# Kernel optimization log

Measured on AMD Instinct MI355X. Metric: run time of the kernel, lower is better.

## Reference

```python
import jax, jax.numpy as jnp
import numpy as np

D_MODEL = 1024
N_HEADS = 16
HEAD_DIM = D_MODEL // N_HEADS
WINDOW = 128
N_PERSIST = 4
KSIZE = 3


def _make_mask(L):
    """[T,T] additive mask, T = N_PERSIST + L. Persistent rows: causal among
    persistent tokens. Sequence rows: all persistent cols + sliding causal window."""
    T = N_PERSIST + L
    r = jnp.arange(T)[:, None]
    c = jnp.arange(T)[None, :]
    seq_allowed = (c < N_PERSIST) | ((c >= jnp.maximum(N_PERSIST, r - WINDOW + 1)) & (c <= r))
    allowed = jnp.where(r < N_PERSIST, c <= r, seq_allowed)
    return jnp.where(allowed, 0.0, -jnp.inf).astype(jnp.float32)


def _causal_dw_conv(y, w, b):
    # y: [B,T,D] -> depthwise causal conv1d + SiLU -> [B,T,D]
    y = y.transpose(0, 2, 1)  # [B,D,T]
    y = jax.lax.conv_general_dilated(
        y, w, window_strides=(1,), padding=[(KSIZE - 1, 0)],
        feature_group_count=D_MODEL, dimension_numbers=('NCH', 'OIH', 'NCH'))
    y = jax.nn.silu(y + b[None, :, None])
    return y.transpose(0, 2, 1)


def _l2norm(y, eps=1e-12):
    n = jnp.linalg.norm(y, axis=-1, keepdims=True)
    return y / jnp.maximum(n, eps)


def setup_inputs() -> dict:
    key = jax.random.key(0)
    ks = jax.random.split(key, 12)
    s = 1.0 / np.sqrt(D_MODEL)
    return {
        'x': jax.random.normal(ks[0], (1, 2048, D_MODEL), jnp.float32),
        'persistent_memory': jax.random.normal(ks[1], (1, N_PERSIST, D_MODEL), jnp.float32) * 0.02,
        'Wq': jax.random.normal(ks[2], (D_MODEL, D_MODEL), jnp.float32) * s,
        'Wk': jax.random.normal(ks[3], (D_MODEL, D_MODEL), jnp.float32) * s,
        'Wv': jax.random.normal(ks[4], (D_MODEL, D_MODEL), jnp.float32) * s,
        'Wo': jax.random.normal(ks[5], (D_MODEL, D_MODEL), jnp.float32) * s,
        'q_conv_w': jax.random.normal(ks[6], (D_MODEL, 1, KSIZE), jnp.float32) * 0.3,
        'q_conv_b': jax.random.normal(ks[7], (D_MODEL,), jnp.float32) * 0.02,
        'k_conv_w': jax.random.normal(ks[8], (D_MODEL, 1, KSIZE), jnp.float32) * 0.3,
        'k_conv_b': jax.random.normal(ks[9], (D_MODEL,), jnp.float32) * 0.02,
        'v_conv_w': jax.random.normal(ks[10], (D_MODEL, 1, KSIZE), jnp.float32) * 0.3,
        'v_conv_b': jax.random.normal(ks[11], (D_MODEL,), jnp.float32) * 0.02,
    }


def reference(x, persistent_memory, Wq, Wk, Wv, Wo,
              q_conv_w, q_conv_b, k_conv_w, k_conv_b, v_conv_w, v_conv_b):
    B, L, D = x.shape
    T = L + N_PERSIST
    scale = HEAD_DIM ** -0.5
    xp = jnp.concatenate([jnp.broadcast_to(persistent_memory, (B, N_PERSIST, D)), x], axis=1)
    Q = xp @ Wq.T
    K = xp @ Wk.T
    V = xp @ Wv.T
    Q = _causal_dw_conv(Q, q_conv_w, q_conv_b)
    K = _causal_dw_conv(K, k_conv_w, k_conv_b)
    V = _causal_dw_conv(V, v_conv_w, v_conv_b)
    Q = _l2norm(Q)
    K = _l2norm(K)
    # [B,H,T,hd]
    Q = Q.reshape(B, T, N_HEADS, HEAD_DIM).transpose(0, 2, 1, 3)
    K = K.reshape(B, T, N_HEADS, HEAD_DIM).transpose(0, 2, 1, 3)
    V = V.reshape(B, T, N_HEADS, HEAD_DIM).transpose(0, 2, 1, 3)
    scores = jnp.einsum('bhqd,bhkd->bhqk', Q, K) * scale + _make_mask(L)[None, None]
    attn = jax.nn.softmax(scores, axis=-1)
    out = jnp.einsum('bhqk,bhkd->bhqd', attn, V)
    out = out.transpose(0, 2, 1, 3).reshape(B, T, D) @ Wo.T
    return out[:, N_PERSIST:, :]
```

## Files before the change

kernel.cpp:

```cpp
#include <hip/hip_runtime.h>
#include <math.h>

typedef unsigned short u16;
typedef unsigned int   u32;
typedef unsigned long long u64;
typedef __attribute__((ext_vector_type(8))) short bf16x8;
typedef __attribute__((ext_vector_type(4))) float f32x4;
typedef __attribute__((ext_vector_type(4))) int i32x4;

#define TTOT  2052
#define NPERS 4
#define LSEQ  2048
#define WIN   128
#define NHEAD 16
#define HDIM  64
#define DM    1024
#define MPAD  2176

__device__ __forceinline__ float bf2f(u16 u) {
    union { unsigned int i; float f; } v; v.i = ((unsigned int)u) << 16; return v.f;
}
__device__ __forceinline__ u16 f2bf(float f) {
    union { float f; unsigned int i; } v; v.f = f;
    unsigned int r = (v.i + 0x7fffu + ((v.i >> 16) & 1u)) >> 16;
    return (u16)r;
}
__device__ __forceinline__ u32 pk2(float lo, float hi) {
    return (u32)f2bf(lo) | ((u32)f2bf(hi) << 16);
}

__device__ __forceinline__ void glds16(const u16* g, u16* l) {
    __builtin_amdgcn_global_load_lds(
        (__attribute__((address_space(1))) void*)(g),
        (__attribute__((address_space(3))) void*)(l),
        16, 0, 0);
}

#define XP_UNITS (TTOT * DM / 4)
#define W_UNITS  (DM * DM / 4)
#define CVT_BLOCKS ((XP_UNITS + 4 * W_UNITS) / 256)

__global__ __launch_bounds__(256) void cvt(const float* __restrict__ x, const float* __restrict__ pm,
    const float* __restrict__ Wq, const float* __restrict__ Wk, const float* __restrict__ Wv,
    const float* __restrict__ Wo,
    u16* __restrict__ xp, u16* __restrict__ Wcat, u16* __restrict__ Woh)
{
    const int id = blockIdx.x * 256 + threadIdx.x;
    const float* s; u16* d;
    if (id < XP_UNITS) {
        const size_t e = (size_t)id * 4;
        const int row = (int)(e >> 10), c = (int)(e & 1023);
        s = (row < NPERS) ? (pm + (size_t)row * DM + c) : (x + (size_t)(row - NPERS) * DM + c);
        d = xp + e;
    } else {
        const int w   = id - XP_UNITS;
        const int sel = w >> 18;
        const size_t e = (size_t)(w & (W_UNITS - 1)) * 4;
        if (sel == 0)      { s = Wq + e; d = Wcat + e; }
        else if (sel == 1) { s = Wk + e; d = Wcat + (size_t)DM * DM + e; }
        else if (sel == 2) { s = Wv + e; d = Wcat + 2 * (size_t)DM * DM + e; }
        else               { s = Wo + e; d = Woh + e; }
    }
    f32x4 v = *(const f32x4*)s;
    *(u64*)d = (u64)pk2(v[0], v[1]) | ((u64)pk2(v[2], v[3]) << 32);
}

template<int TM, int TN, bool OF32>
__device__ __forceinline__ void gemm_lds(const u16* __restrict__ Ablk, const u16* __restrict__ Bblk,
                                         void* __restrict__ Cbase, int mlim)
{
    __shared__ __align__(16) u16 As[TM * 64];
    __shared__ __align__(16) u16 Bs[TN * 64];
    const int tid  = threadIdx.x;
    const int lane = tid & 63;
    const int l15  = lane & 15, quad = lane >> 4;
    constexpr int RM = TM / 32, RN = TN / 32;
    const int wm = (tid >> 7) * (TM / 2);
    const int wn = ((tid >> 6) & 1) * (TN / 2);

    f32x4 acc[RM][RN];
    #pragma unroll
    for (int i = 0; i < RM; i++)
        #pragma unroll
        for (int j = 0; j < RN; j++) acc[i][j] = (f32x4){0.f, 0.f, 0.f, 0.f};

    constexpr int LA = TM / 32;
    constexpr int LB = TN / 32;

    for (int kk = 0; kk < DM; kk += 64) {
        #pragma unroll
        for (int i = 0; i < LA; i++) {
            const int e = i * 256 + tid;
            const int row = e >> 3, sc = (e & 7) ^ (row & 7);
            glds16(Ablk + (size_t)row * DM + kk + sc * 8, As + (size_t)e * 8);
        }
        #pragma unroll
        for (int i = 0; i < LB; i++) {
            const int e = i * 256 + tid;
            const int row = e >> 3, sc = (e & 7) ^ (row & 7);
            glds16(Bblk + (size_t)row * DM + kk + sc * 8, Bs + (size_t)e * 8);
        }
        __syncthreads();
        #pragma unroll
        for (int kc = 0; kc < 2; kc++) {
            bf16x8 af[RM], bfr[RN];
            #pragma unroll
            for (int i = 0; i < RM; i++)
                af[i]  = *(const bf16x8*)&As[(wm + i * 16 + l15) * 64 + (((kc * 4 + quad) ^ (l15 & 7)) * 8)];
            #pragma unroll
            for (int j = 0; j < RN; j++)
                bfr[j] = *(const bf16x8*)&Bs[(wn + j * 16 + l15) * 64 + (((kc * 4 + quad) ^ (l15 & 7)) * 8)];
            #pragma unroll
            for (int i = 0; i < RM; i++)
                #pragma unroll
                for (int j = 0; j < RN; j++)
                    acc[i][j] = __builtin_amdgcn_mfma_f32_16x16x32_bf16(af[i], bfr[j], acc[i][j], 0, 0, 0);
        }
        __syncthreads();
    }

    #pragma unroll
    for (int i = 0; i < RM; i++) {
        const int m0 = wm + i * 16 + quad * 4;
        #pragma unroll
        for (int j = 0; j < RN; j++) {
            const int n = wn + j * 16 + l15;
            #pragma unroll
            for (int r = 0; r < 4; r++) {
                const int m = m0 + r;
                if (m < mlim) {
                    if (OF32) ((float*)Cbase)[(size_t)m * DM + n] = acc[i][j][r];
                    else      ((u16*)Cbase)[(size_t)m * DM + n]   = f2bf(acc[i][j][r]);
                }
            }
        }
    }
}

__global__ __launch_bounds__(256) void gemm_qkv(const u16* __restrict__ xp, const u16* __restrict__ Wcat,
    u16* __restrict__ Qr, u16* __restrict__ Kr, u16* __restrict__ Vr)
{
    const int Mb = blockIdx.x * 128;
    const int nb = blockIdx.y;
    u16* C = (nb < 8) ? Qr : (nb < 16) ? Kr : Vr;
    const int Ncol = (nb & 7) * 128;
    gemm_lds<128, 128, false>(xp + (size_t)Mb * DM,
                              Wcat + (size_t)nb * 128 * DM,
                              (void*)(C + (size_t)Mb * DM + Ncol),
                              TTOT - Mb);
}

__global__ __launch_bounds__(256) void gemm_out(const u16* __restrict__ AO, const u16* __restrict__ Woh,
                                                float* __restrict__ Cout)
{
    const int Mb = blockIdx.x * 64, Nb = blockIdx.y * 128;
    gemm_lds<64, 128, true>(AO + (size_t)Mb * DM, Woh + (size_t)Nb * DM,
                            (void*)(Cout + (size_t)Mb * DM + Nb), 64);
}

__global__ __launch_bounds__(256) void conv_silu_norm(
    const u16* __restrict__ Qr, const u16* __restrict__ Kr, const u16* __restrict__ Vr,
    const float* __restrict__ qw, const float* __restrict__ qb,
    const float* __restrict__ kw, const float* __restrict__ kb,
    const float* __restrict__ vw, const float* __restrict__ vb,
    u16* __restrict__ Qc, u16* __restrict__ Kc, u16* __restrict__ Vc)
{
    const int t0 = blockIdx.x * 2;
    const int z  = blockIdx.y;
    const u16* raw; const float *w, *b; u16* out;
    if (z == 0)      { raw = Qr; w = qw; b = qb; out = Qc; }
    else if (z == 1) { raw = Kr; w = kw; b = kb; out = Kc; }
    else             { raw = Vr; w = vw; b = vb; out = Vc; }

    const int tid = threadIdx.x;
    const int d0  = tid * 4;

    const u16* r0 = raw + (size_t)t0 * DM + d0;
    const u64 cm2 = (t0 >= 2) ? *(const u64*)(r0 - 2 * DM) : 0ULL;
    const u64 cm1 = (t0 >= 1) ? *(const u64*)(r0 - DM)     : 0ULL;
    const u64 c0  = *(const u64*)r0;
    const u64 c1  = *(const u64*)(r0 + DM);
    const f32x4 bias = *(const f32x4*)(b + d0);
    const f32x4 w0v  = *(const f32x4*)(w + 3 * d0);
    const f32x4 w1v  = *(const f32x4*)(w + 3 * d0 + 4);
    const f32x4 w2v  = *(const f32x4*)(w + 3 * d0 + 8);
    const float warr[12] = {w0v[0], w0v[1], w0v[2], w0v[3],
                            w1v[0], w1v[1], w1v[2], w1v[3],
                            w2v[0], w2v[1], w2v[2], w2v[3]};

    float va[4], vb2[4];
    float ss0 = 0.f, ss1 = 0.f;
    #pragma unroll
    for (int c = 0; c < 4; c++) {
        const float xm2 = bf2f((u16)(cm2 >> (16 * c)));
        const float xm1 = bf2f((u16)(cm1 >> (16 * c)));
        const float x0  = bf2f((u16)(c0  >> (16 * c)));
        const float x1  = bf2f((u16)(c1  >> (16 * c)));
        const float w0 = warr[3*c], w1 = warr[3*c + 1], w2 = warr[3*c + 2];
        float a0 = bias[c] + w2 * x0 + w1 * xm1 + w0 * xm2;
        float a1 = bias[c] + w2 * x1 + w1 * x0  + w0 * xm1;
        const float y0 = a0 / (1.f + __expf(-a0));
        const float y1 = a1 / (1.f + __expf(-a1));
        va[c] = y0; vb2[c] = y1;
        ss0 += y0 * y0; ss1 += y1 * y1;
    }
    float inv0 = 1.f, inv1 = 1.f;
    if (z < 2) {
        #pragma unroll
        for (int off = 32; off > 0; off >>= 1) {
            ss0 += __shfl_down(ss0, off, 64);
            ss1 += __shfl_down(ss1, off, 64);
        }
        __shared__ float red[8];
        const int wv = tid >> 6, ln = tid & 63;
        if (ln == 0) { red[wv] = ss0; red[wv + 4] = ss1; }
        __syncthreads();
        inv0 = 1.f / fmaxf(sqrtf(red[0] + red[1] + red[2] + red[3]), 1e-12f);
        inv1 = 1.f / fmaxf(sqrtf(red[4] + red[5] + red[6] + red[7]), 1e-12f);
    }
    u64 o0 = 0, o1 = 0;
    #pragma unroll
    for (int c = 0; c < 4; c++) {
        o0 |= (u64)f2bf(va[c]  * inv0) << (16 * c);
        o1 |= (u64)f2bf(vb2[c] * inv1) << (16 * c);
    }
    *(u64*)(out + (size_t)t0 * DM + d0)      = o0;
    *(u64*)(out + (size_t)(t0 + 1) * DM + d0) = o1;
}

#define QT     64
#define KTILES 13
#define KROWS  208
#define KPAD   224
#define VSTR   232

__global__ __launch_bounds__(256) void attn(const u16* __restrict__ Q, const u16* __restrict__ K,
                                            const u16* __restrict__ V, u16* __restrict__ AO)
{
    const int h  = blockIdx.y;
    const int qb = blockIdx.x * QT;
    const int kstart = max(NPERS, qb + NPERS - (WIN - 1));
    const int nk = NPERS + (qb + NPERS + QT - 1) - kstart + 1;

    __shared__ __align__(16) u16 KP[64 * VSTR];
    __shared__ __align__(16) u16 Vt[64 * VSTR];
    u16* Ks = KP;
    u16* Ps = KP;

    const int tid  = threadIdx.x;
    const int wv   = tid >> 6, lane = tid & 63, l15 = lane & 15, quad = lane >> 4;

    u32 vreg[28];
    #pragma unroll
    for (int i = 0; i < 28; i++) {
        const int i2 = wv * 2 + i * 8;
        const int g0 = (i2     < NPERS) ? i2     : min(kstart + i2     - NPERS, TTOT - 1);
        const int g1 = (i2 + 1 < NPERS) ? i2 + 1 : min(kstart + i2 + 1 - NPERS, TTOT - 1);
        vreg[i] = (u32)V[(size_t)g0 * DM + h * HDIM + lane]
                | ((u32)V[(size_t)g1 * DM + h * HDIM + lane] << 16);
    }

    #pragma unroll
    for (int i = 0; i < 7; i++) {
        const int c = i * 256 + tid;
        if (c < KROWS * 8) {
            const int r  = c >> 3;
            const int sc = (c & 7) ^ (r & 7);
            const int g  = (r < NPERS) ? r : min(kstart + r - NPERS, TTOT - 1);
            glds16(K + (size_t)g * DM + h * HDIM + sc * 8, Ks + (size_t)c * 8);
        }
    }
    __syncthreads();

    const int qloc0 = wv * 16;
    const int tqrow = qb + qloc0 + l15 + NPERS;
    const bf16x8 qa0 = *(const bf16x8*)&Q[(size_t)tqrow * DM + h * HDIM + quad * 8];
    const bf16x8 qa1 = *(const bf16x8*)&Q[(size_t)tqrow * DM + h * HDIM + 32 + quad * 8];

    const int sw = l15 & 7;
    f32x4 st[KTILES];
    #pragma unroll
    for (int t = 0; t < KTILES; t++) {
        const bf16x8 kb0 = *(const bf16x8*)&Ks[(t * 16 + l15) * 64 + ((quad ^ sw) * 8)];
        const bf16x8 kb1 = *(const bf16x8*)&Ks[(t * 16 + l15) * 64 + (((4 + quad) ^ sw) * 8)];
        f32x4 z = (f32x4){0.f, 0.f, 0.f, 0.f};
        z = __builtin_amdgcn_mfma_f32_16x16x32_bf16(qa0, kb0, z, 0, 0, 0);
        z = __builtin_amdgcn_mfma_f32_16x16x32_bf16(qa1, kb1, z, 0, 0, 0);
        st[t] = z;
    }

    const float scale = 0.125f;
    float ssum[4] = {0.f, 0.f, 0.f, 0.f};
    #pragma unroll
    for (int t = 0; t < KTILES; t++) {
        const int i  = t * 16 + l15;
        const int kg = kstart + i - NPERS;
        #pragma unroll
        for (int r = 0; r < 4; r++) {
            const int tqr = qb + qloc0 + quad * 4 + r + NPERS;
            const bool ok = (i < NPERS) || ((i < nk) && (kg >= tqr - (WIN - 1)) && (kg <= tqr));
            const float p = ok ? __expf(st[t][r] * scale) : 0.f;
            st[t][r] = p;
            ssum[r] += p;
        }
    }
    #pragma unroll
    for (int off = 1; off < 16; off <<= 1)
        #pragma unroll
        for (int r = 0; r < 4; r++) ssum[r] += __shfl_xor(ssum[r], off, 64);
    float inv[4];
    #pragma unroll
    for (int r = 0; r < 4; r++) inv[r] = 1.f / ssum[r];

    __syncthreads();

    #pragma unroll
    for (int i = 0; i < 28; i++) {
        const int i2 = wv * 2 + i * 8;
        *(u32*)&Vt[lane * VSTR + i2] = vreg[i];
    }
    #pragma unroll
    for (int t = 0; t < KTILES; t++)
        #pragma unroll
        for (int r = 0; r < 4; r++)
            Ps[(qloc0 + quad * 4 + r) * VSTR + t * 16 + l15] = f2bf(st[t][r] * inv[r]);
    *(u64*)&Ps[(qloc0 + l15) * VSTR + KROWS + quad * 4] = 0ULL;
    __syncthreads();

    f32x4 oacc[4];
    #pragma unroll
    for (int dt = 0; dt < 4; dt++) oacc[dt] = (f32x4){0.f, 0.f, 0.f, 0.f};
    for (int ks = 0; ks < KPAD / 32; ks++) {
        const bf16x8 pa = *(const bf16x8*)&Ps[(qloc0 + l15) * VSTR + ks * 32 + quad * 8];
        #pragma unroll
        for (int dt = 0; dt < 4; dt++) {
            const bf16x8 vb = *(const bf16x8*)&Vt[(dt * 16 + l15) * VSTR + ks * 32 + quad * 8];
            oacc[dt] = __builtin_amdgcn_mfma_f32_16x16x32_bf16(pa, vb, oacc[dt], 0, 0, 0);
        }
    }

    #pragma unroll
    for (int dt = 0; dt < 4; dt++)
        #pragma unroll
        for (int r = 0; r < 4; r++)
            AO[(size_t)(qb + qloc0 + quad * 4 + r) * DM + h * HDIM + dt * 16 + l15] = f2bf(oacc[dt][r]);
}

extern "C" void kernel_launch(void* const* d_in, const int* in_sizes, int n_in,
                              void* d_out, int out_size, void* d_ws, size_t ws_size,
                              hipStream_t stream)
{
    const float* x  = (const float*)d_in[0];
    const float* pm = (const float*)d_in[1];
    const float* Wq = (const float*)d_in[2];
    const float* Wk = (const float*)d_in[3];
    const float* Wv = (const float*)d_in[4];
    const float* Wo = (const float*)d_in[5];
    const float* qw = (const float*)d_in[6];
    const float* qb = (const float*)d_in[7];
    const float* kw = (const float*)d_in[8];
    const float* kb = (const float*)d_in[9];
    const float* vw = (const float*)d_in[10];
    const float* vb = (const float*)d_in[11];
    float* out = (float*)d_out;

    u16* ws16 = (u16*)d_ws;
    const size_t SZ_W  = (size_t)DM * DM;
    const size_t SZ_R  = (size_t)TTOT * DM;
    const size_t SZ_XP = (size_t)MPAD * DM;
    u16* Woh  = ws16;
    u16* Qr   = Woh + SZ_W;        u16* AO = Qr;
    u16* Kr   = Qr + SZ_R;
    u16* Vr   = Kr + SZ_R;
    u16* Vc   = Vr + SZ_R;
    u16* xp   = Vc + SZ_R;         u16* Qc = xp;
    u16* Wcat = xp + SZ_XP;        u16* Kc = Wcat;

    hipLaunchKernelGGL(cvt, dim3(CVT_BLOCKS), dim3(256), 0, stream,
                       x, pm, Wq, Wk, Wv, Wo, xp, Wcat, Woh);
    hipLaunchKernelGGL(gemm_qkv, dim3(17, 24), dim3(256), 0, stream,
                       xp, Wcat, Qr, Kr, Vr);
    hipLaunchKernelGGL(conv_silu_norm, dim3(TTOT / 2, 3), dim3(256), 0, stream,
                       Qr, Kr, Vr, qw, qb, kw, kb, vw, vb, Qc, Kc, Vc);
    hipLaunchKernelGGL(attn, dim3(LSEQ / QT, NHEAD), dim3(256), 0, stream,
                       Qc, Kc, Vc, AO);
    hipLaunchKernelGGL(gemm_out, dim3(32, 8), dim3(256), 0, stream,
                       AO, Woh, out);
}
```

Baseline: 150.0 us.

## Fuse QKV GEMM with causal conv+SiLU and defer L2 norm into attention

Replaces the separate QKV GEMM and conv/SiLU/norm kernels with one kernel that computes overlapping 128-row tiles (126 useful rows plus 2 halo rows) and applies the depthwise conv and SiLU from shared memory. Row sums of squares for Q and K are accumulated with atomics into a buffer, and attention applies the inverse norms to the scores. This removes one launch and the raw Q/K/V round trip through global memory. In exchange it recomputes halo rows, issues many per-row atomics and a 63-step serial epilogue loop, and changes rounding because unnormalized bf16 values feed the MFMA.

```diff
diff --git a/kernel.cpp b/kernel.cpp
--- a/kernel.cpp
+++ b/kernel.cpp
@@ -16,6 +16,7 @@
 #define HDIM  64
 #define DM    1024
 #define MPAD  2176
+#define MSTEP 126
 
 __device__ __forceinline__ float bf2f(u16 u) {
     union { unsigned int i; float f; } v; v.i = ((unsigned int)u) << 16; return v.f;
@@ -43,9 +44,11 @@
 __global__ __launch_bounds__(256) void cvt(const float* __restrict__ x, const float* __restrict__ pm,
     const float* __restrict__ Wq, const float* __restrict__ Wk, const float* __restrict__ Wv,
     const float* __restrict__ Wo,
-    u16* __restrict__ xp, u16* __restrict__ Wcat, u16* __restrict__ Woh)
+    u16* __restrict__ xp, u16* __restrict__ Wcat, u16* __restrict__ Woh,
+    float* __restrict__ nsq)
 {
     const int id = blockIdx.x * 256 + threadIdx.x;
+    if (id < 2 * TTOT) nsq[id] = 0.f;
     const float* s; u16* d;
     if (id < XP_UNITS) {
         const size_t e = (size_t)id * 4;
@@ -137,19 +140,6 @@
     }
 }
 
-__global__ __launch_bounds__(256) void gemm_qkv(const u16* __restrict__ xp, const u16* __restrict__ Wcat,
-    u16* __restrict__ Qr, u16* __restrict__ Kr, u16* __restrict__ Vr)
-{
-    const int Mb = blockIdx.x * 128;
-    const int nb = blockIdx.y;
-    u16* C = (nb < 8) ? Qr : (nb < 16) ? Kr : Vr;
-    const int Ncol = (nb & 7) * 128;
-    gemm_lds<128, 128, false>(xp + (size_t)Mb * DM,
-                              Wcat + (size_t)nb * 128 * DM,
-                              (void*)(C + (size_t)Mb * DM + Ncol),
-                              TTOT - Mb);
-}
-
 __global__ __launch_bounds__(256) void gemm_out(const u16* __restrict__ AO, const u16* __restrict__ Woh,
                                                 float* __restrict__ Cout)
 {
@@ -158,74 +148,105 @@
                             (void*)(Cout + (size_t)Mb * DM + Nb), 64);
 }
 
-__global__ __launch_bounds__(256) void conv_silu_norm(
-    const u16* __restrict__ Qr, const u16* __restrict__ Kr, const u16* __restrict__ Vr,
+__global__ __launch_bounds__(256) void gemm_qkv_conv(
+    const u16* __restrict__ xp, const u16* __restrict__ Wcat,
     const float* __restrict__ qw, const float* __restrict__ qb,
     const float* __restrict__ kw, const float* __restrict__ kb,
     const float* __restrict__ vw, const float* __restrict__ vb,
-    u16* __restrict__ Qc, u16* __restrict__ Kc, u16* __restrict__ Vc)
-{
-    const int t0 = blockIdx.x * 2;
-    const int z  = blockIdx.y;
-    const u16* raw; const float *w, *b; u16* out;
-    if (z == 0)      { raw = Qr; w = qw; b = qb; out = Qc; }
-    else if (z == 1) { raw = Kr; w = kw; b = kb; out = Kc; }
-    else             { raw = Vr; w = vw; b = vb; out = Vc; }
-
-    const int tid = threadIdx.x;
-    const int d0  = tid * 4;
-
-    const u16* r0 = raw + (size_t)t0 * DM + d0;
-    const u64 cm2 = (t0 >= 2) ? *(const u64*)(r0 - 2 * DM) : 0ULL;
-    const u64 cm1 = (t0 >= 1) ? *(const u64*)(r0 - DM)     : 0ULL;
-    const u64 c0  = *(const u64*)r0;
-    const u64 c1  = *(const u64*)(r0 + DM);
-    const f32x4 bias = *(const f32x4*)(b + d0);
-    const f32x4 w0v  = *(const f32x4*)(w + 3 * d0);
-    const f32x4 w1v  = *(const f32x4*)(w + 3 * d0 + 4);
-    const f32x4 w2v  = *(const f32x4*)(w + 3 * d0 + 8);
-    const float warr[12] = {w0v[0], w0v[1], w0v[2], w0v[3],
-                            w1v[0], w1v[1], w1v[2], w1v[3],
-                            w2v[0], w2v[1], w2v[2], w2v[3]};
-
-    float va[4], vb2[4];
-    float ss0 = 0.f, ss1 = 0.f;
-    #pragma unroll
-    for (int c = 0; c < 4; c++) {
-        const float xm2 = bf2f((u16)(cm2 >> (16 * c)));
-        const float xm1 = bf2f((u16)(cm1 >> (16 * c)));
-        const float x0  = bf2f((u16)(c0  >> (16 * c)));
-        const float x1  = bf2f((u16)(c1  >> (16 * c)));
-        const float w0 = warr[3*c], w1 = warr[3*c + 1], w2 = warr[3*c + 2];
-        float a0 = bias[c] + w2 * x0 + w1 * xm1 + w0 * xm2;
-        float a1 = bias[c] + w2 * x1 + w1 * x0  + w0 * xm1;
-        const float y0 = a0 / (1.f + __expf(-a0));
-        const float y1 = a1 / (1.f + __expf(-a1));
-        va[c] = y0; vb2[c] = y1;
-        ss0 += y0 * y0; ss1 += y1 * y1;
-    }
-    float inv0 = 1.f, inv1 = 1.f;
-    if (z < 2) {
-        #pragma unroll
-        for (int off = 32; off > 0; off >>= 1) {
-            ss0 += __shfl_down(ss0, off, 64);
-            ss1 += __shfl_down(ss1, off, 64);
-        }
-        __shared__ float red[8];
-        const int wv = tid >> 6, ln = tid & 63;
-        if (ln == 0) { red[wv] = ss0; red[wv + 4] = ss1; }
+    u16* __restrict__ Qc, u16* __restrict__ Kc, u16* __restrict__ Vc,
+    float* __restrict__ nsq)
+{
+    __shared__ __align__(16) u16 buf[128 * 129];
+    u16* As = buf;
+    u16* Bs = buf + 8192;
+
+    const int tid  = threadIdx.x;
+    const int lane = tid & 63;
+    const int l15  = lane & 15, quad = lane >> 4;
+    const int wm = (tid >> 7) * 64;
+    const int wn = ((tid >> 6) & 1) * 64;
+
+    const int bx = blockIdx.x;
+    const int nb = blockIdx.y;
+    const int Mh = bx * MSTEP - 2;
+    const u16* Bblk = Wcat + (size_t)nb * 128 * DM;
+
+    f32x4 acc[4][4];
+    #pragma unroll
+    for (int i = 0; i < 4; i++)
+        #pragma unroll
+        for (int j = 0; j < 4; j++) acc[i][j] = (f32x4){0.f, 0.f, 0.f, 0.f};
+
+    for (int kk = 0; kk < DM; kk += 64) {
+        #pragma unroll
+        for (int i = 0; i < 4; i++) {
+            const int e = i * 256 + tid;
+            const int row = e >> 3, sc = (e & 7) ^ (row & 7);
+            const int mg = max(Mh + row, 0);
+            glds16(xp + (size_t)mg * DM + kk + sc * 8, As + (size_t)e * 8);
+        }
+        #pragma unroll
+        for (int i = 0; i < 4; i++) {
+            const int e = i * 256 + tid;
+            const int row = e >> 3, sc = (e & 7) ^ (row & 7);
+            glds16(Bblk + (size_t)row * DM + kk + sc * 8, Bs + (size_t)e * 8);
+        }
         __syncthreads();
-        inv0 = 1.f / fmaxf(sqrtf(red[0] + red[1] + red[2] + red[3]), 1e-12f);
-        inv1 = 1.f / fmaxf(sqrtf(red[4] + red[5] + red[6] + red[7]), 1e-12f);
-    }
-    u64 o0 = 0, o1 = 0;
-    #pragma unroll
-    for (int c = 0; c < 4; c++) {
-        o0 |= (u64)f2bf(va[c]  * inv0) << (16 * c);
-        o1 |= (u64)f2bf(vb2[c] * inv1) << (16 * c);
-    }
-    *(u64*)(out + (size_t)t0 * DM + d0)      = o0;
-    *(u64*)(out + (size_t)(t0 + 1) * DM + d0) = o1;
+        #pragma unroll
+        for (int kc = 0; kc < 2; kc++) {
+            bf16x8 af[4], bfr[4];
+            #pragma unroll
+            for (int i = 0; i < 4; i++)
+                af[i]  = *(const bf16x8*)&As[(wm + i * 16 + l15) * 64 + (((kc * 4 + quad) ^ (l15 & 7)) * 8)];
+            #pragma unroll
+            for (int j = 0; j < 4; j++)
+                bfr[j] = *(const bf16x8*)&Bs[(wn + j * 16 + l15) * 64 + (((kc * 4 + quad) ^ (l15 & 7)) * 8)];
+            #pragma unroll
+            for (int i = 0; i < 4; i++)
+                #pragma unroll
+                for (int j = 0; j < 4; j++)
+                    acc[i][j] = __builtin_amdgcn_mfma_f32_16x16x32_bf16(af[i], bfr[j], acc[i][j], 0, 0, 0);
+        }
+        __syncthreads();
+    }
+
+    #pragma unroll
+    for (int i = 0; i < 4; i++)
+        #pragma unroll
+        for (int j = 0; j < 4; j++)
+            #pragma unroll
+            for (int r = 0; r < 4; r++)
+                buf[(wm + i * 16 + quad * 4 + r) * 129 + (wn + j * 16 + l15)] = f2bf(acc[i][j][r]);
+    __syncthreads();
+
+    const int part = nb >> 3;
+    const int c    = tid & 127;
+    const int ch   = (nb & 7) * 128 + c;
+    const int half = tid >> 7;
+    const float *w, *b; u16* dst;
+    if (part == 0)      { w = qw; b = qb; dst = Qc; }
+    else if (part == 1) { w = kw; b = kb; dst = Kc; }
+    else                { w = vw; b = vb; dst = Vc; }
+    const float w0 = w[ch * 3], w1 = w[ch * 3 + 1], w2 = w[ch * 3 + 2], bb = b[ch];
+    float* nrow = nsq + part * TTOT;
+
+    for (int k = 0; k < 63; k++) {
+        const int rloc = 2 + k * 2 + half;
+        const int t = Mh + rloc;
+        if (t >= TTOT) break;
+        const float x0  = bf2f(buf[rloc * 129 + c]);
+        const float xm1 = (t >= 1) ? bf2f(buf[(rloc - 1) * 129 + c]) : 0.f;
+        const float xm2 = (t >= 2) ? bf2f(buf[(rloc - 2) * 129 + c]) : 0.f;
+        const float a = bb + w2 * x0 + w1 * xm1 + w0 * xm2;
+        const float y = a / (1.f + __expf(-a));
+        dst[(size_t)t * DM + ch] = f2bf(y);
+        if (part < 2) {
+            float ss = y * y;
+            #pragma unroll
+            for (int off = 32; off > 0; off >>= 1) ss += __shfl_down(ss, off, 64);
+            if (lane == 0) atomicAdd(nrow + t, ss);
+        }
+    }
 }
 
 #define QT     64
@@ -235,7 +256,8 @@
 #define VSTR   232
 
 __global__ __launch_bounds__(256) void attn(const u16* __restrict__ Q, const u16* __restrict__ K,
-                                            const u16* __restrict__ V, u16* __restrict__ AO)
+                                            const u16* __restrict__ V, const float* __restrict__ nsq,
+                                            u16* __restrict__ AO)
 {
     const int h  = blockIdx.y;
     const int qb = blockIdx.x * QT;
@@ -249,6 +271,7 @@
 
     const int tid  = threadIdx.x;
     const int wv   = tid >> 6, lane = tid & 63, l15 = lane & 15, quad = lane >> 4;
+    const int qloc0 = wv * 16;
 
     u32 vreg[28];
     #pragma unroll
@@ -259,20 +282,29 @@
         vreg[i] = (u32)V[(size_t)g0 * DM + h * HDIM + lane]
                 | ((u32)V[(size_t)g1 * DM + h * HDIM + lane] << 16);
     }
+    float kss[KTILES];
+    #pragma unroll
+    for (int t = 0; t < KTILES; t++) {
+        const int i = t * 16 + l15;
+        const int gk = (i < NPERS) ? i : min(kstart + i - NPERS, TTOT - 1);
+        kss[t] = nsq[TTOT + gk];
+    }
+    float qss[4];
+    #pragma unroll
+    for (int r = 0; r < 4; r++) qss[r] = nsq[qb + qloc0 + quad * 4 + r + NPERS];
 
     #pragma unroll
     for (int i = 0; i < 7; i++) {
-        const int c = i * 256 + tid;
-        if (c < KROWS * 8) {
-            const int r  = c >> 3;
-            const int sc = (c & 7) ^ (r & 7);
+        const int cdx = i * 256 + tid;
+        if (cdx < KROWS * 8) {
+            const int r  = cdx >> 3;
+            const int sc = (cdx & 7) ^ (r & 7);
             const int g  = (r < NPERS) ? r : min(kstart + r - NPERS, TTOT - 1);
-            glds16(K + (size_t)g * DM + h * HDIM + sc * 8, Ks + (size_t)c * 8);
+            glds16(K + (size_t)g * DM + h * HDIM + sc * 8, Ks + (size_t)cdx * 8);
         }
     }
     __syncthreads();
 
-    const int qloc0 = wv * 16;
     const int tqrow = qb + qloc0 + l15 + NPERS;
     const bf16x8 qa0 = *(const bf16x8*)&Q[(size_t)tqrow * DM + h * HDIM + quad * 8];
     const bf16x8 qa1 = *(const bf16x8*)&Q[(size_t)tqrow * DM + h * HDIM + 32 + quad * 8];
@@ -290,16 +322,20 @@
     }
 
     const float scale = 0.125f;
+    float iq[4];
+    #pragma unroll
+    for (int r = 0; r < 4; r++) iq[r] = scale / fmaxf(sqrtf(qss[r]), 1e-12f);
     float ssum[4] = {0.f, 0.f, 0.f, 0.f};
     #pragma unroll
     for (int t = 0; t < KTILES; t++) {
         const int i  = t * 16 + l15;
         const int kg = kstart + i - NPERS;
+        const float ik = 1.f / fmaxf(sqrtf(kss[t]), 1e-12f);
         #pragma unroll
         for (int r = 0; r < 4; r++) {
             const int tqr = qb + qloc0 + quad * 4 + r + NPERS;
             const bool ok = (i < NPERS) || ((i < nk) && (kg >= tqr - (WIN - 1)) && (kg <= tqr));
-            const float p = ok ? __expf(st[t][r] * scale) : 0.f;
+            const float p = ok ? __expf(st[t][r] * ik * iq[r]) : 0.f;
             st[t][r] = p;
             ssum[r] += p;
         }
@@ -369,21 +405,19 @@
     const size_t SZ_R  = (size_t)TTOT * DM;
     const size_t SZ_XP = (size_t)MPAD * DM;
     u16* Woh  = ws16;
-    u16* Qr   = Woh + SZ_W;        u16* AO = Qr;
-    u16* Kr   = Qr + SZ_R;
-    u16* Vr   = Kr + SZ_R;
-    u16* Vc   = Vr + SZ_R;
-    u16* xp   = Vc + SZ_R;         u16* Qc = xp;
-    u16* Wcat = xp + SZ_XP;        u16* Kc = Wcat;
+    u16* Qc   = Woh + SZ_W;
+    u16* Kc   = Qc + SZ_R;
+    u16* Vc   = Kc + SZ_R;
+    u16* xp   = Vc + SZ_R;         u16* AO = xp;
+    u16* Wcat = xp + SZ_XP;
+    float* nsq = (float*)(Wcat + 3 * SZ_W);
 
     hipLaunchKernelGGL(cvt, dim3(CVT_BLOCKS), dim3(256), 0, stream,
-                       x, pm, Wq, Wk, Wv, Wo, xp, Wcat, Woh);
-    hipLaunchKernelGGL(gemm_qkv, dim3(17, 24), dim3(256), 0, stream,
-                       xp, Wcat, Qr, Kr, Vr);
-    hipLaunchKernelGGL(conv_silu_norm, dim3(TTOT / 2, 3), dim3(256), 0, stream,
-                       Qr, Kr, Vr, qw, qb, kw, kb, vw, vb, Qc, Kc, Vc);
+                       x, pm, Wq, Wk, Wv, Wo, xp, Wcat, Woh, nsq);
+    hipLaunchKernelGGL(gemm_qkv_conv, dim3(17, 24), dim3(256), 0, stream,
+                       xp, Wcat, qw, qb, kw, kb, vw, vb, Qc, Kc, Vc, nsq);
     hipLaunchKernelGGL(attn, dim3(LSEQ / QT, NHEAD), dim3(256), 0, stream,
-                       Qc, Kc, Vc, AO);
+                       Qc, Kc, Vc, nsq, AO);
     hipLaunchKernelGGL(gemm_out, dim3(32, 8), dim3(256), 0, stream,
                        AO, Woh, out);
 }
```

After: 167.5 us. 1.12x slower.
